# Performance work log

Hardware: AMD Instinct MI355X
Metric: run time of the kernel (lower is better)

## Reference

```python
import jax, jax.numpy as jnp
import numpy as np

NEG_SLOPE = 0.2  # PyG GATConv default negative_slope


def setup_inputs() -> dict:
    key = jax.random.key(0)
    k_x, k_e, k_w, k_as, k_ad = jax.random.split(key, 5)
    B, F, N, D, E, L = 2, 16, 5000, 128, 40000, 3
    x = jax.random.normal(k_x, (B, F, N, D), dtype=jnp.float32)
    edge_index = jax.random.randint(k_e, (B, F, 2, E), 0, N, dtype=jnp.int64)
    Ws = jax.random.normal(k_w, (L, D, D), dtype=jnp.float32) / np.float32(np.sqrt(D))
    att_src = jax.random.normal(k_as, (L, D), dtype=jnp.float32) / np.float32(np.sqrt(D))
    att_dst = jax.random.normal(k_ad, (L, D), dtype=jnp.float32) / np.float32(np.sqrt(D))
    bias = jnp.zeros((L, D), dtype=jnp.float32)
    return {"x": x, "edge_index": edge_index, "Ws": Ws,
            "att_src": att_src, "att_dst": att_dst, "bias": bias}


def _gat_layer(h, src, dst, n, W, a_s, a_d, b):
    # h: [n, D] node features; src/dst: [E_tot] edge endpoints (self-loops included)
    h2 = h @ W                                   # [n, D] transformed features
    s = h2 @ a_s                                 # [n] per-node source score
    d = h2 @ a_d                                 # [n] per-node dest score
    e = jax.nn.leaky_relu(s[src] + d[dst], NEG_SLOPE)   # [E_tot] raw attention
    m = jax.lax.stop_gradient(jax.ops.segment_max(e, dst, num_segments=n))
    ex = jnp.exp(e - m[dst])                     # numerically stable softmax per dst
    denom = jax.ops.segment_sum(ex, dst, num_segments=n)
    alpha = ex / denom[dst]                      # [E_tot] normalized attention
    out = jax.ops.segment_sum(alpha[:, None] * h2[src], dst, num_segments=n) + b
    return jax.nn.relu(out)


def reference(x, edge_index, Ws, att_src, att_dst, bias):
    B, F, N, D = x.shape
    n = B * F * N
    h = x.reshape(n, D)
    # faithful to torch: (BF,2,E).view(2,-1) is a raw row-major reshape
    ei = edge_index.reshape(2, -1)
    loop = jnp.arange(n, dtype=ei.dtype)         # PyG GATConv adds self-loops
    src = jnp.concatenate([ei[0], loop])
    dst = jnp.concatenate([ei[1], loop])
    for l in range(Ws.shape[0]):                 # fixed small layer loop
        h = _gat_layer(h, src, dst, n, Ws[l], att_src[l], att_dst[l], bias[l])
    return h.reshape(B, F, N, D)
```

## Files before the change

### kernel.cpp

```cpp
#include <hip/hip_runtime.h>
#include <math.h>

#define NODES_TOTAL 160000
#define NODES_REAL  5000
#define D 128
#define NEG 0.2f
#define KP2 128
#define HL2 (128 * KP2)
#define WT2_L (2 * HL2)
#define CHUNK 16384

typedef unsigned short ushort_t;
typedef unsigned int uint_t;
typedef __attribute__((ext_vector_type(8))) __bf16 bf16x8;
typedef __attribute__((ext_vector_type(4))) float f32x4;
union BF8 { bf16x8 v; ushort_t u[8]; };

__device__ __forceinline__ void split2(float x, ushort_t& hi, ushort_t& lo) {
    unsigned u = __float_as_uint(x);
    hi = (ushort_t)(u >> 16);
    float hif = __uint_as_float(u & 0xffff0000u);
    lo = (ushort_t)(__float_as_uint(x - hif) >> 16);
}
__device__ __forceinline__ uint_t encmax(float f) {
    uint_t b = __float_as_uint(f);
    return b ^ ((uint_t)((int)b >> 31) | 0x80000000u);
}
__device__ __forceinline__ float decmax(uint_t u) {
    uint_t b = (u & 0x80000000u) ? (u ^ 0x80000000u) : ~u;
    return __uint_as_float(b);
}

__global__ void wsplit_kernel(const float* __restrict__ Ws, ushort_t* __restrict__ Wm,
                              int* __restrict__ counts, uint_t* __restrict__ gmaxu) {
    int gid = blockIdx.x * 256 + threadIdx.x;
    if (gid < NODES_REAL) counts[gid] = 0;
    if (gid < 3) gmaxu[gid] = 0u;
    int l  = blockIdx.x >> 3;
    int n  = (blockIdx.x & 7) * 16 + (threadIdx.x >> 4);
    int c8 = threadIdx.x & 15;
    int k0 = c8 * 8;
    const float* src = Ws + (size_t)l * D * D;
    union { ushort_t u[8]; uint4 v; } hi, lo;
    #pragma unroll
    for (int j = 0; j < 8; ++j) split2(src[(size_t)(k0 + j) * D + n], hi.u[j], lo.u[j]);
    int ct = n >> 4, m16 = n & 15, kc = c8 >> 2, qq = c8 & 3;
    int lane = qq * 16 + m16;
    ushort_t* d2 = Wm + (size_t)l * WT2_L + ((ct * 4 + kc) * 2 + 0) * 512 + lane * 8;
    *(uint4*)d2 = hi.v;
    *(uint4*)(d2 + 512) = lo.v;
}

__device__ __forceinline__ void mlp3_body(const float* __restrict__ x,
        const ushort_t* __restrict__ Wm, const float* __restrict__ bs,
        float* __restrict__ out, int row_base, int bid, int tid,
        float (*scr)[2][16][132]) {
    int w = tid >> 6, lane = tid & 63, q = lane >> 4, m16 = lane & 15;
    int p = w >> 1, h = w & 1;
    int row0 = row_base + bid * 64 + p * 32;

    float4 xa[2][4][2];
    #pragma unroll
    for (int rt = 0; rt < 2; ++rt) {
        int r = row0 + rt * 16 + m16;
        if (r > NODES_TOTAL - 1) r = NODES_TOTAL - 1;
        #pragma unroll
        for (int kc = 0; kc < 4; ++kc) {
            const float* gp = x + (size_t)r * D + kc * 32 + q * 8;
            xa[rt][kc][0] = *(const float4*)gp;
            xa[rt][kc][1] = *(const float4*)(gp + 4);
        }
    }

    f32x4 acc[2][4];
    #pragma unroll
    for (int l = 0; l < 3; ++l) {
        const ushort_t* Wml = Wm + (size_t)l * WT2_L;
        if (l > 0) __syncthreads();

        BF8 ahi[2][4], alo[2][4];
        #pragma unroll
        for (int rt = 0; rt < 2; ++rt)
            #pragma unroll
            for (int kc = 0; kc < 4; ++kc) {
                float4 v0, v1;
                if (l == 0) { v0 = xa[rt][kc][0]; v1 = xa[rt][kc][1]; }
                else {
                    const float* sp = &scr[p][rt][m16][kc * 32 + q * 8];
                    v0 = *(const float4*)sp; v1 = *(const float4*)(sp + 4);
                }
                float xv[8] = {v0.x, v0.y, v0.z, v0.w, v1.x, v1.y, v1.z, v1.w};
                #pragma unroll
                for (int j = 0; j < 8; ++j) split2(xv[j], ahi[rt][kc].u[j], alo[rt][kc].u[j]);
            }
        if (l > 0) __syncthreads();

        #pragma unroll
        for (int rt = 0; rt < 2; ++rt)
            #pragma unroll
            for (int ct = 0; ct < 4; ++ct) acc[rt][ct] = (f32x4){0.f, 0.f, 0.f, 0.f};

        #pragma unroll
        for (int ph = 0; ph < 2; ++ph) {
            int kc0 = ph * 2;
            bf16x8 bh[4][2], bl[4][2];
            #pragma unroll
            for (int ct = 0; ct < 4; ++ct)
                #pragma unroll
                for (int dk = 0; dk < 2; ++dk) {
                    const ushort_t* bp = Wml + (((h * 4 + ct) * 4 + (kc0 + dk)) * 2) * 512 + lane * 8;
                    bh[ct][dk] = *(const bf16x8*)bp;
                    bl[ct][dk] = *(const bf16x8*)(bp + 512);
                }
            #pragma unroll
            for (int dk = 0; dk < 2; ++dk)
                #pragma unroll
                for (int ct = 0; ct < 4; ++ct)
                    #pragma unroll
                    for (int rt = 0; rt < 2; ++rt) {
                        acc[rt][ct] = __builtin_amdgcn_mfma_f32_16x16x32_bf16(ahi[rt][kc0 + dk].v, bh[ct][dk], acc[rt][ct], 0, 0, 0);
                        acc[rt][ct] = __builtin_amdgcn_mfma_f32_16x16x32_bf16(ahi[rt][kc0 + dk].v, bl[ct][dk], acc[rt][ct], 0, 0, 0);
                        acc[rt][ct] = __builtin_amdgcn_mfma_f32_16x16x32_bf16(alo[rt][kc0 + dk].v, bh[ct][dk], acc[rt][ct], 0, 0, 0);
                    }
        }
        float bv[4];
        #pragma unroll
        for (int ct = 0; ct < 4; ++ct) bv[ct] = bs[l * D + (h * 4 + ct) * 16 + m16];
        #pragma unroll
        for (int rt = 0; rt < 2; ++rt)
            #pragma unroll
            for (int ct = 0; ct < 4; ++ct)
                #pragma unroll
                for (int reg = 0; reg < 4; ++reg)
                    scr[p][rt][q * 4 + reg][(h * 4 + ct) * 16 + m16] =
                        fmaxf(acc[rt][ct][reg] + bv[ct], 0.f);
    }
    __syncthreads();
    #pragma unroll
    for (int i = 0; i < 8; ++i) {
        int rowl = i * 2 + (lane >> 5);
        int grow = row0 + h * 16 + rowl;
        float4 v = *(const float4*)&scr[p][h][rowl][(lane & 31) * 4];
        if (grow < NODES_TOTAL)
            *(float4*)&out[(size_t)grow * D + (lane & 31) * 4] = v;
    }
}

__device__ __forceinline__ void gsmall_wave(const float* __restrict__ hin,
        const ushort_t* __restrict__ Wml, const float* __restrict__ a_s,
        const float* __restrict__ a_d, float* __restrict__ h2,
        float* __restrict__ sv, float* __restrict__ dv, uint_t* __restrict__ gmax,
        int row0, int lane) {
    int q = lane >> 4, m16 = lane & 15;
    int rr = row0 + m16; if (rr > NODES_REAL - 1) rr = NODES_REAL - 1;
    f32x4 acc[8];
    #pragma unroll
    for (int ct = 0; ct < 8; ++ct) acc[ct] = (f32x4){0.f, 0.f, 0.f, 0.f};
    #pragma unroll
    for (int kc = 0; kc < 4; ++kc) {
        const float* gp = hin + (size_t)rr * D + kc * 32 + q * 8;
        float4 v0 = *(const float4*)gp, v1 = *(const float4*)(gp + 4);
        BF8 ahi, alo;
        {
            float xv[8] = {v0.x, v0.y, v0.z, v0.w, v1.x, v1.y, v1.z, v1.w};
            #pragma unroll
            for (int j = 0; j < 8; ++j) split2(xv[j], ahi.u[j], alo.u[j]);
        }
        #pragma unroll
        for (int cth = 0; cth < 2; ++cth) {
            bf16x8 bh[4], bl[4];
            #pragma unroll
            for (int c4 = 0; c4 < 4; ++c4) {
                int ct = cth * 4 + c4;
                const ushort_t* bp = Wml + ((ct * 4 + kc) * 2) * 512 + lane * 8;
                bh[c4] = *(const bf16x8*)bp;
                bl[c4] = *(const bf16x8*)(bp + 512);
            }
            #pragma unroll
            for (int c4 = 0; c4 < 4; ++c4) {
                int ct = cth * 4 + c4;
                acc[ct] = __builtin_amdgcn_mfma_f32_16x16x32_bf16(ahi.v, bh[c4], acc[ct], 0, 0, 0);
                acc[ct] = __builtin_amdgcn_mfma_f32_16x16x32_bf16(ahi.v, bl[c4], acc[ct], 0, 0, 0);
                acc[ct] = __builtin_amdgcn_mfma_f32_16x16x32_bf16(alo.v, bh[c4], acc[ct], 0, 0, 0);
            }
        }
    }
    #pragma unroll
    for (int reg = 0; reg < 4; ++reg) {
        int grow = row0 + q * 4 + reg;
        if (grow < NODES_REAL) {
            #pragma unroll
            for (int ct = 0; ct < 8; ++ct)
                h2[(size_t)grow * D + ct * 16 + m16] = acc[ct][reg];
        }
    }
    float asv[8], adv[8];
    #pragma unroll
    for (int ct = 0; ct < 8; ++ct) { asv[ct] = a_s[ct * 16 + m16]; adv[ct] = a_d[ct * 16 + m16]; }
    #pragma unroll
    for (int reg = 0; reg < 4; ++reg) {
        float ps = 0.f, pd = 0.f;
        #pragma unroll
        for (int ct = 0; ct < 8; ++ct) {
            float v = acc[ct][reg];
            ps += v * asv[ct]; pd += v * adv[ct];
        }
        #pragma unroll
        for (int o = 1; o < 16; o <<= 1) { ps += __shfl_xor(ps, o); pd += __shfl_xor(pd, o); }
        int grow = row0 + q * 4 + reg;
        if (m16 == 0 && grow < NODES_REAL) {
            sv[grow] = ps; dv[grow] = pd;
            atomicMax(gmax, encmax(ps));
        }
    }
}

__device__ __forceinline__ void agg_dst(int i, const float* __restrict__ h2,
        const float* __restrict__ sv, const float* __restrict__ dv,
        const int* __restrict__ offs, const ushort_t* __restrict__ esrc,
        const float* __restrict__ bias, float* __restrict__ hout,
        const uint_t* __restrict__ gmaxu, int w, int lane, int tid,
        float2* pair_l, float2 (*red)[64], float* lexs) {
    int start = offs[i], end = offs[i + 1];
    float d_i = dv[i];
    float gm = decmax(*gmaxu) + d_i;
    float m = gm > 0.f ? gm : NEG * gm;
    const float2* h2v = (const float2*)h2;
    float ax0 = 0.f, ay0 = 0.f, ax1 = 0.f, ay1 = 0.f;
    float ax2 = 0.f, ay2 = 0.f, ax3 = 0.f, ay3 = 0.f, exs = 0.f;
    for (int tile = start; tile < end; tile += 512) {
        int tcnt = min(512, end - tile);
        __syncthreads();
        #pragma unroll
        for (int hh = 0; hh < 2; ++hh) {
            int j = hh * 256 + tid;
            if (j < tcnt) {
                int s = (int)esrc[tile + j];
                float sc = sv[s] + d_i;
                sc = sc > 0.f ? sc : NEG * sc;
                float ex = __expf(sc - m);
                exs += ex;
                pair_l[j] = make_float2(ex, __uint_as_float((uint_t)s));
            }
        }
        __syncthreads();
        for (int j0 = w * 64; j0 < tcnt; j0 += 256) {
            int jend = min(j0 + 64, tcnt);
            int j = j0;
            for (; j + 4 <= jend; j += 4) {
                float2 p0 = pair_l[j],     p1 = pair_l[j + 1];
                float2 p2 = pair_l[j + 2], p3 = pair_l[j + 3];
                float2 v0 = h2v[(size_t)__float_as_uint(p0.y) * 64 + lane];
                float2 v1 = h2v[(size_t)__float_as_uint(p1.y) * 64 + lane];
                float2 v2 = h2v[(size_t)__float_as_uint(p2.y) * 64 + lane];
                float2 v3 = h2v[(size_t)__float_as_uint(p3.y) * 64 + lane];
                ax0 += p0.x * v0.x; ay0 += p0.x * v0.y;
                ax1 += p1.x * v1.x; ay1 += p1.x * v1.y;
                ax2 += p2.x * v2.x; ay2 += p2.x * v2.y;
                ax3 += p3.x * v3.x; ay3 += p3.x * v3.y;
            }
            for (; j < jend; ++j) {
                float2 p0 = pair_l[j];
                float2 v0 = h2v[(size_t)__float_as_uint(p0.y) * 64 + lane];
                ax0 += p0.x * v0.x; ay0 += p0.x * v0.y;
            }
        }
    }
    float ax = (ax0 + ax1) + (ax2 + ax3);
    float ay = (ay0 + ay1) + (ay2 + ay3);
    #pragma unroll
    for (int o = 1; o < 64; o <<= 1) exs += __shfl_xor(exs, o);
    __syncthreads();
    red[w][lane] = make_float2(ax, ay);
    if (lane == 0) lexs[w] = exs;
    __syncthreads();
    if (w == 0) {
        float2 r1 = red[1][lane], r2 = red[2][lane], r3 = red[3][lane];
        ax += r1.x + r2.x + r3.x;
        ay += r1.y + r2.y + r3.y;
        float exst = lexs[0] + lexs[1] + lexs[2] + lexs[3];
        float scf = sv[i] + d_i; scf = scf > 0.f ? scf : NEG * scf;
        float exf = __expf(scf - m);
        float2 hv = h2v[(size_t)i * 64 + lane];
        ax += exf * hv.x; ay += exf * hv.y;
        float rd = 1.f / (exst + exf);
        float2 b2 = *(const float2*)&bias[2 * lane];
        float2 o2 = make_float2(fmaxf(ax * rd + b2.x, 0.f), fmaxf(ay * rd + b2.y, 0.f));
        *(float2*)&hout[(size_t)i * D + 2 * lane] = o2;
    }
}

__global__ __launch_bounds__(256, 4)
void comboA_kernel(const int* __restrict__ ei, int* __restrict__ counts,
                   int* __restrict__ bases, ushort_t* __restrict__ rank16,
                   int Eh, int nchunks,
                   const float* __restrict__ x, const ushort_t* __restrict__ Wm,
                   const float* __restrict__ as_, const float* __restrict__ ad_,
                   float* __restrict__ h2, float* __restrict__ sv,
                   float* __restrict__ dv, uint_t* __restrict__ gmaxu) {
    __shared__ uint_t lc[NODES_REAL];
    int b = blockIdx.x, tid = threadIdx.x;
    if (b < nchunks) {
        for (int i2 = tid; i2 < NODES_REAL; i2 += 256) lc[i2] = 0u;
        __syncthreads();
        int e0 = b * CHUNK;
        #pragma unroll 4
        for (int k = 0; k < CHUNK / 256; ++k) {
            int e = e0 + k * 256 + tid;
            if (e < Eh) {
                int d = ei[Eh + e];
                uint_t r = atomicAdd(&lc[d], 1u);
                rank16[e] = (ushort_t)r;
            }
        }
        __syncthreads();
        for (int i2 = tid; i2 < NODES_REAL; i2 += 256) {
            uint_t n = lc[i2];
            if (n > 0u)
                bases[b * NODES_REAL + i2] = atomicAdd(&counts[i2], (int)n);
        }
    } else {
        int gw = (b - nchunks) * 4 + (tid >> 6);
        if (gw * 16 < NODES_REAL)
            gsmall_wave(x, Wm, as_, ad_, h2, sv, dv, gmaxu + 0, gw * 16, tid & 63);
    }
}

__global__ void scan_kernel(const int* __restrict__ counts, int* __restrict__ offs) {
    __shared__ int sd[1024];
    int t = threadIdx.x;
    int pre[5]; int sum = 0;
    #pragma unroll
    for (int u = 0; u < 5; ++u) {
        int idx = t * 5 + u;
        int c = (idx < NODES_REAL) ? counts[idx] : 0;
        pre[u] = sum; sum += c;
    }
    sd[t] = sum;
    __syncthreads();
    int run = sum;
    for (int o = 1; o < 1024; o <<= 1) {
        int v = (t >= o) ? sd[t - o] : 0;
        __syncthreads();
        sd[t] += v;
        __syncthreads();
    }
    int excl = sd[t] - run;
    #pragma unroll
    for (int u = 0; u < 5; ++u) {
        int idx = t * 5 + u;
        if (idx < NODES_REAL) offs[idx] = excl + pre[u];
    }
    if (t == 1023) offs[NODES_REAL] = excl + run;
}

__global__ void scatter_det(const int* __restrict__ ei, const int* __restrict__ offs,
                            const int* __restrict__ bases,
                            const ushort_t* __restrict__ rank16, ushort_t* __restrict__ esrc,
                            int Eh) {
    int e = blockIdx.x * blockDim.x + threadIdx.x;
    if (e < Eh) {
        int s = ei[e];
        int d = ei[Eh + e];
        int c = e >> 14;
        esrc[offs[d] + bases[c * NODES_REAL + d] + (int)rank16[e]] = (ushort_t)s;
    }
}

__global__ __launch_bounds__(256, 2)
void combo_kernel(const float* __restrict__ x, const ushort_t* __restrict__ Wm,
                  const float* __restrict__ bs, float* __restrict__ out,
                  int mlp_nb, int mlp_row_base,
                  const float* __restrict__ h2, const float* __restrict__ sv,
                  const float* __restrict__ dv, const int* __restrict__ offs,
                  const ushort_t* __restrict__ esrc, const float* __restrict__ bias_l,
                  float* __restrict__ hout, const uint_t* __restrict__ gmaxu_l) {
    __shared__ float scr[2][2][16][132];
    __shared__ float2 pair_l[512];
    __shared__ float2 red[4][64];
    __shared__ float lexs[4];
    int b = blockIdx.x, tid = threadIdx.x;
    if (b < mlp_nb) {
        mlp3_body(x, Wm, bs, out, mlp_row_base, b, tid, scr);
    } else {
        int i = b - mlp_nb;
        agg_dst(i, h2, sv, dv, offs, esrc, bias_l, hout, gmaxu_l,
                tid >> 6, tid & 63, tid, pair_l, red, lexs);
    }
}

__global__ __launch_bounds__(64, 2)
void gsmall_kernel(const float* __restrict__ hin, const ushort_t* __restrict__ Wm,
                   const float* __restrict__ a_s, const float* __restrict__ a_d,
                   float* __restrict__ h2, float* __restrict__ sv, float* __restrict__ dv,
                   uint_t* __restrict__ gmaxu) {
    gsmall_wave(hin, Wm, a_s, a_d, h2, sv, dv, gmaxu, blockIdx.x * 16, threadIdx.x & 63);
}

extern "C" void kernel_launch(void* const* d_in, const int* in_sizes, int n_in,
                              void* d_out, int out_size, void* d_ws, size_t ws_size,
                              hipStream_t stream) {
    const float* x   = (const float*)d_in[0];
    const int*   ei  = (const int*)d_in[1];
    const float* Ws  = (const float*)d_in[2];
    const float* as_ = (const float*)d_in[3];
    const float* ad_ = (const float*)d_in[4];
    const float* bs  = (const float*)d_in[5];
    float* out = (float*)d_out;
    int Eh = in_sizes[1] / 2;
    int nchunks = (Eh + CHUNK - 1) / CHUNK;

    char* ws = (char*)d_ws;
    float*    h2     = (float*)ws;
    float*    bufS   = (float*)(ws + 2560000);
    float*    sv     = (float*)(ws + 5120000);
    float*    dv     = (float*)(ws + 5140000);
    int*      counts = (int*)  (ws + 5160000);
    int*      offs   = (int*)  (ws + 5180000);
    ushort_t* rank16 = (ushort_t*)(ws + 5200016);
    ushort_t* esrc   = (ushort_t*)(ws + 7760016);
    ushort_t* Wm     = (ushort_t*)(ws + 10320016);
    uint_t*   gmaxu  = (uint_t*)(ws + 10528912);
    int*      bases  = (int*)bufS;

    const int MLP_NB = (NODES_TOTAL - NODES_REAL + 63) / 64;
    const int S0 = 808, S1 = 808, S2 = MLP_NB - S0 - S1;

    wsplit_kernel<<<24, 256, 0, stream>>>(Ws, Wm, counts, gmaxu);
    comboA_kernel<<<nchunks + (NODES_REAL + 63) / 64, 256, 0, stream>>>(
        ei, counts, bases, rank16, Eh, nchunks, x, Wm, as_, ad_, h2, sv, dv, gmaxu);
    scan_kernel<<<1, 1024, 0, stream>>>(counts, offs);
    scatter_det<<<(Eh + 255) / 256, 256, 0, stream>>>(ei, offs, bases, rank16, esrc, Eh);

    combo_kernel<<<S0 + NODES_REAL, 256, 0, stream>>>(
        x, Wm, bs, out, S0, NODES_REAL + 0 * 64,
        h2, sv, dv, offs, esrc, bs + 0 * D, bufS, gmaxu + 0);
    gsmall_kernel<<<(NODES_REAL + 15) / 16, 64, 0, stream>>>(
        bufS, Wm + WT2_L, as_ + D, ad_ + D, h2, sv, dv, gmaxu + 1);
    combo_kernel<<<S1 + NODES_REAL, 256, 0, stream>>>(
        x, Wm, bs, out, S1, NODES_REAL + S0 * 64,
        h2, sv, dv, offs, esrc, bs + 1 * D, bufS, gmaxu + 1);
    gsmall_kernel<<<(NODES_REAL + 15) / 16, 64, 0, stream>>>(
        bufS, Wm + 2 * WT2_L, as_ + 2 * D, ad_ + 2 * D, h2, sv, dv, gmaxu + 2);
    combo_kernel<<<S2 + NODES_REAL, 256, 0, stream>>>(
        x, Wm, bs, out, S2, NODES_REAL + (S0 + S1) * 64,
        h2, sv, dv, offs, esrc, bs + 2 * D, out, gmaxu + 2);
}
```

Before: 477.7 us.

## Split MLP work into own kernel and aggregate one destination per wavefront

```diff
diff --git a/kernel.cpp b/kernel.cpp
--- a/kernel.cpp
+++ b/kernel.cpp
@@ -146,6 +146,13 @@
     }
 }
 
+__global__ __launch_bounds__(256, 2)
+void mlp3_kernel(const float* __restrict__ x, const ushort_t* __restrict__ Wm,
+                 const float* __restrict__ bs, float* __restrict__ out) {
+    __shared__ float scr[2][2][16][132];
+    mlp3_body(x, Wm, bs, out, NODES_REAL, blockIdx.x, threadIdx.x, scr);
+}
+
 __device__ __forceinline__ void gsmall_wave(const float* __restrict__ hin,
         const ushort_t* __restrict__ Wml, const float* __restrict__ a_s,
         const float* __restrict__ a_d, float* __restrict__ h2,
@@ -212,81 +219,6 @@
             sv[grow] = ps; dv[grow] = pd;
             atomicMax(gmax, encmax(ps));
         }
-    }
-}
-
-__device__ __forceinline__ void agg_dst(int i, const float* __restrict__ h2,
-        const float* __restrict__ sv, const float* __restrict__ dv,
-        const int* __restrict__ offs, const ushort_t* __restrict__ esrc,
-        const float* __restrict__ bias, float* __restrict__ hout,
-        const uint_t* __restrict__ gmaxu, int w, int lane, int tid,
-        float2* pair_l, float2 (*red)[64], float* lexs) {
-    int start = offs[i], end = offs[i + 1];
-    float d_i = dv[i];
-    float gm = decmax(*gmaxu) + d_i;
-    float m = gm > 0.f ? gm : NEG * gm;
-    const float2* h2v = (const float2*)h2;
-    float ax0 = 0.f, ay0 = 0.f, ax1 = 0.f, ay1 = 0.f;
-    float ax2 = 0.f, ay2 = 0.f, ax3 = 0.f, ay3 = 0.f, exs = 0.f;
-    for (int tile = start; tile < end; tile += 512) {
-        int tcnt = min(512, end - tile);
-        __syncthreads();
-        #pragma unroll
-        for (int hh = 0; hh < 2; ++hh) {
-            int j = hh * 256 + tid;
-            if (j < tcnt) {
-                int s = (int)esrc[tile + j];
-                float sc = sv[s] + d_i;
-                sc = sc > 0.f ? sc : NEG * sc;
-                float ex = __expf(sc - m);
-                exs += ex;
-                pair_l[j] = make_float2(ex, __uint_as_float((uint_t)s));
-            }
-        }
-        __syncthreads();
-        for (int j0 = w * 64; j0 < tcnt; j0 += 256) {
-            int jend = min(j0 + 64, tcnt);
-            int j = j0;
-            for (; j + 4 <= jend; j += 4) {
-                float2 p0 = pair_l[j],     p1 = pair_l[j + 1];
-                float2 p2 = pair_l[j + 2], p3 = pair_l[j + 3];
-                float2 v0 = h2v[(size_t)__float_as_uint(p0.y) * 64 + lane];
-                float2 v1 = h2v[(size_t)__float_as_uint(p1.y) * 64 + lane];
-                float2 v2 = h2v[(size_t)__float_as_uint(p2.y) * 64 + lane];
-                float2 v3 = h2v[(size_t)__float_as_uint(p3.y) * 64 + lane];
-                ax0 += p0.x * v0.x; ay0 += p0.x * v0.y;
-                ax1 += p1.x * v1.x; ay1 += p1.x * v1.y;
-                ax2 += p2.x * v2.x; ay2 += p2.x * v2.y;
-                ax3 += p3.x * v3.x; ay3 += p3.x * v3.y;
-            }
-            for (; j < jend; ++j) {
-                float2 p0 = pair_l[j];
-                float2 v0 = h2v[(size_t)__float_as_uint(p0.y) * 64 + lane];
-                ax0 += p0.x * v0.x; ay0 += p0.x * v0.y;
-            }
-        }
-    }
-    float ax = (ax0 + ax1) + (ax2 + ax3);
-    float ay = (ay0 + ay1) + (ay2 + ay3);
-    #pragma unroll
-    for (int o = 1; o < 64; o <<= 1) exs += __shfl_xor(exs, o);
-    __syncthreads();
-    red[w][lane] = make_float2(ax, ay);
-    if (lane == 0) lexs[w] = exs;
-    __syncthreads();
-    if (w == 0) {
-        float2 r1 = red[1][lane], r2 = red[2][lane], r3 = red[3][lane];
-        ax += r1.x + r2.x + r3.x;
-        ay += r1.y + r2.y + r3.y;
-        float exst = lexs[0] + lexs[1] + lexs[2] + lexs[3];
-        float scf = sv[i] + d_i; scf = scf > 0.f ? scf : NEG * scf;
-        float exf = __expf(scf - m);
-        float2 hv = h2v[(size_t)i * 64 + lane];
-        ax += exf * hv.x; ay += exf * hv.y;
-        float rd = 1.f / (exst + exf);
-        float2 b2 = *(const float2*)&bias[2 * lane];
-        float2 o2 = make_float2(fmaxf(ax * rd + b2.x, 0.f), fmaxf(ay * rd + b2.y, 0.f));
-        *(float2*)&hout[(size_t)i * D + 2 * lane] = o2;
     }
 }
 
@@ -367,26 +299,68 @@
     }
 }
 
-__global__ __launch_bounds__(256, 2)
-void combo_kernel(const float* __restrict__ x, const ushort_t* __restrict__ Wm,
-                  const float* __restrict__ bs, float* __restrict__ out,
-                  int mlp_nb, int mlp_row_base,
-                  const float* __restrict__ h2, const float* __restrict__ sv,
-                  const float* __restrict__ dv, const int* __restrict__ offs,
-                  const ushort_t* __restrict__ esrc, const float* __restrict__ bias_l,
-                  float* __restrict__ hout, const uint_t* __restrict__ gmaxu_l) {
-    __shared__ float scr[2][2][16][132];
-    __shared__ float2 pair_l[512];
-    __shared__ float2 red[4][64];
-    __shared__ float lexs[4];
-    int b = blockIdx.x, tid = threadIdx.x;
-    if (b < mlp_nb) {
-        mlp3_body(x, Wm, bs, out, mlp_row_base, b, tid, scr);
-    } else {
-        int i = b - mlp_nb;
-        agg_dst(i, h2, sv, dv, offs, esrc, bias_l, hout, gmaxu_l,
-                tid >> 6, tid & 63, tid, pair_l, red, lexs);
-    }
+__global__ __launch_bounds__(256, 4)
+void agg_kernel(const float* __restrict__ h2, const float* __restrict__ sv,
+                const float* __restrict__ dv, const int* __restrict__ offs,
+                const ushort_t* __restrict__ esrc, const float* __restrict__ bias,
+                float* __restrict__ out, const uint_t* __restrict__ gmaxu) {
+    __shared__ float2 pair[4][64];
+    int tid = threadIdx.x, w = tid >> 6, lane = tid & 63;
+    int i = blockIdx.x * 4 + w;
+    int start = offs[i], end = offs[i + 1];
+    float d_i = dv[i];
+    float gm = decmax(*gmaxu) + d_i;
+    float m = gm > 0.f ? gm : NEG * gm;
+    const float2* h2v = (const float2*)h2;
+    float ax[8], ay[8];
+    #pragma unroll
+    for (int t = 0; t < 8; ++t) { ax[t] = 0.f; ay[t] = 0.f; }
+    float exs = 0.f;
+    for (int base = start; base < end; base += 64) {
+        int cnt = min(64, end - base);
+        int srci = 0; float ex = 0.f;
+        if (lane < cnt) {
+            srci = (int)esrc[base + lane];
+            float sc = sv[srci] + d_i;
+            sc = sc > 0.f ? sc : NEG * sc;
+            ex = __expf(sc - m);
+        }
+        exs += ex;
+        pair[w][lane] = make_float2(ex, __uint_as_float((uint_t)srci));
+        if (cnt == 64) {
+            #pragma unroll
+            for (int j = 0; j < 64; j += 8) {
+                float2 p[8], v[8];
+                #pragma unroll
+                for (int t = 0; t < 8; ++t) p[t] = pair[w][j + t];
+                #pragma unroll
+                for (int t = 0; t < 8; ++t)
+                    v[t] = h2v[(size_t)__float_as_uint(p[t].y) * 64 + lane];
+                #pragma unroll
+                for (int t = 0; t < 8; ++t) {
+                    ax[t] += p[t].x * v[t].x; ay[t] += p[t].x * v[t].y;
+                }
+            }
+        } else {
+            for (int j = 0; j < cnt; ++j) {
+                float2 p0 = pair[w][j];
+                float2 v0 = h2v[(size_t)__float_as_uint(p0.y) * 64 + lane];
+                ax[0] += p0.x * v0.x; ay[0] += p0.x * v0.y;
+            }
+        }
+    }
+    float axs = ((ax[0] + ax[1]) + (ax[2] + ax[3])) + ((ax[4] + ax[5]) + (ax[6] + ax[7]));
+    float ays = ((ay[0] + ay[1]) + (ay[2] + ay[3])) + ((ay[4] + ay[5]) + (ay[6] + ay[7]));
+    #pragma unroll
+    for (int o = 1; o < 64; o <<= 1) exs += __shfl_xor(exs, o);
+    float scf = sv[i] + d_i; scf = scf > 0.f ? scf : NEG * scf;
+    float exf = __expf(scf - m);
+    float2 hv = h2v[(size_t)i * 64 + lane];
+    axs += exf * hv.x; ays += exf * hv.y;
+    float rd = 1.f / (exs + exf);
+    float2 b2 = *(const float2*)&bias[2 * lane];
+    float2 o2 = make_float2(fmaxf(axs * rd + b2.x, 0.f), fmaxf(ays * rd + b2.y, 0.f));
+    *(float2*)&out[(size_t)i * D + 2 * lane] = o2;
 }
 
 __global__ __launch_bounds__(64, 2)
@@ -423,26 +397,22 @@
     uint_t*   gmaxu  = (uint_t*)(ws + 10528912);
     int*      bases  = (int*)bufS;
 
-    const int MLP_NB = (NODES_TOTAL - NODES_REAL + 63) / 64;
-    const int S0 = 808, S1 = 808, S2 = MLP_NB - S0 - S1;
-
     wsplit_kernel<<<24, 256, 0, stream>>>(Ws, Wm, counts, gmaxu);
     comboA_kernel<<<nchunks + (NODES_REAL + 63) / 64, 256, 0, stream>>>(
         ei, counts, bases, rank16, Eh, nchunks, x, Wm, as_, ad_, h2, sv, dv, gmaxu);
     scan_kernel<<<1, 1024, 0, stream>>>(counts, offs);
     scatter_det<<<(Eh + 255) / 256, 256, 0, stream>>>(ei, offs, bases, rank16, esrc, Eh);
 
-    combo_kernel<<<S0 + NODES_REAL, 256, 0, stream>>>(
-        x, Wm, bs, out, S0, NODES_REAL + 0 * 64,
+    mlp3_kernel<<<(NODES_TOTAL - NODES_REAL + 63) / 64, 256, 0, stream>>>(x, Wm, bs, out);
+
+    agg_kernel<<<NODES_REAL / 4, 256, 0, stream>>>(
         h2, sv, dv, offs, esrc, bs + 0 * D, bufS, gmaxu + 0);
     gsmall_kernel<<<(NODES_REAL + 15) / 16, 64, 0, stream>>>(
         bufS, Wm + WT2_L, as_ + D, ad_ + D, h2, sv, dv, gmaxu + 1);
-    combo_kernel<<<S1 + NODES_REAL, 256, 0, stream>>>(
-        x, Wm, bs, out, S1, NODES_REAL + S0 * 64,
+    agg_kernel<<<NODES_REAL / 4, 256, 0, stream>>>(
         h2, sv, dv, offs, esrc, bs + 1 * D, bufS, gmaxu + 1);
     gsmall_kernel<<<(NODES_REAL + 15) / 16, 64, 0, stream>>>(
         bufS, Wm + 2 * WT2_L, as_ + 2 * D, ad_ + 2 * D, h2, sv, dv, gmaxu + 2);
-    combo_kernel<<<S2 + NODES_REAL, 256, 0, stream>>>(
-        x, Wm, bs, out, S2, NODES_REAL + (S0 + S1) * 64,
+    agg_kernel<<<NODES_REAL / 4, 256, 0, stream>>>(
         h2, sv, dv, offs, esrc, bs + 2 * D, out, gmaxu + 2);
 }
```

Measured after the change: 486.8 us. About the same (+1.9%).
